# Optimization experiments

Hardware: AMD Instinct MI355X
Metric: run time of the kernel (lower is better)

Reference implementation:

```python
import jax, jax.numpy as jnp
import numpy as np

B, S, D, H = 2, 2048, 512, 8


def setup_inputs() -> dict:
    key = jax.random.key(0)
    ks = jax.random.split(key, 9)
    scale = 1.0 / np.sqrt(D)
    x = jax.random.normal(ks[0], (B, S, D), dtype=jnp.float32)
    # Per-head full-width projections, stacked over heads: [H, D, D]
    Wq = jax.random.normal(ks[1], (H, D, D), dtype=jnp.float32) * scale
    Wk = jax.random.normal(ks[2], (H, D, D), dtype=jnp.float32) * scale
    Wv = jax.random.normal(ks[3], (H, D, D), dtype=jnp.float32) * scale
    bq = jax.random.normal(ks[4], (H, D), dtype=jnp.float32) * 0.01
    bk = jax.random.normal(ks[5], (H, D), dtype=jnp.float32) * 0.01
    bv = jax.random.normal(ks[6], (H, D), dtype=jnp.float32) * 0.01
    Wo = jax.random.normal(ks[7], (H * D, D), dtype=jnp.float32) * (1.0 / np.sqrt(H * D))
    bo = jax.random.normal(ks[8], (D,), dtype=jnp.float32) * 0.01
    return {"x": x, "Wq": Wq, "bq": bq, "Wk": Wk, "bk": bk, "Wv": Wv, "bv": bv, "Wo": Wo, "bo": bo}


def reference(x, Wq, bq, Wk, bk, Wv, bv, Wo, bo):
    # Batched per-head projections: [B,S,D] x [H,D,E] -> [B,H,S,E]
    q = jnp.einsum('bsd,hde->bhse', x, Wq) + bq[None, :, None, :]
    k = jnp.einsum('bsd,hde->bhse', x, Wk) + bk[None, :, None, :]
    v = jnp.einsum('bsd,hde->bhse', x, Wv) + bv[None, :, None, :]
    # NOTE: original module has NO 1/sqrt(d) scaling
    scores = jnp.einsum('bhse,bhte->bhst', q, k)  # [B,H,S,S]
    attn = jax.nn.softmax(scores, axis=-1)
    out = jnp.einsum('bhst,bhte->bhse', attn, v)  # [B,H,S,D]
    # Concat heads along feature dim: [B,S,H*D]
    cat = out.transpose(0, 2, 1, 3).reshape(B, S, H * D)
    return cat @ Wo + bo
```

## Files before the change

kernel.cpp:

```cpp
#include <hip/hip_runtime.h>

typedef _Float16 f16;
typedef _Float16 f16x8 __attribute__((ext_vector_type(8)));
typedef float f32x4 __attribute__((ext_vector_type(4)));

#define B_ 2
#define S_ 2048
#define D_ 512
#define H_ 8

__device__ inline void async_ld16(const void* g, void* l) {
  __builtin_amdgcn_global_load_lds((__attribute__((address_space(1))) void*)(g),
                                   (__attribute__((address_space(3))) void*)(l),
                                   16, 0, 0);
}

__global__ __launch_bounds__(256) void cvt_f16(const float* __restrict__ src,
                                               f16* __restrict__ dst, long n) {
  long i = (long)blockIdx.x * 256 + threadIdx.x;
  if (i >= n) return;
  dst[i] = (f16)src[i];
}

__global__ __launch_bounds__(256) void transpose_f32(const float* __restrict__ src,
                                                     f16* __restrict__ dst, int R, int C) {
  __shared__ float t[32][33];
  size_t zoff = (size_t)blockIdx.z * R * C;
  const float* s = src + zoff;
  int tx = threadIdx.x;
  int ty = threadIdx.y;
  int c0 = blockIdx.x * 32, r0 = blockIdx.y * 32;
#pragma unroll
  for (int i = 0; i < 4; ++i)
    t[ty + i * 8][tx] = s[(size_t)(r0 + ty + i * 8) * C + c0 + tx];
  __syncthreads();
#pragma unroll
  for (int i = 0; i < 4; ++i)
    dst[zoff + (size_t)(c0 + ty + i * 8) * R + r0 + tx] = (f16)t[tx][ty + i * 8];
}

__global__ __launch_bounds__(256) void reduce_out(const float* __restrict__ part,
                                                  const float* __restrict__ bo,
                                                  float* __restrict__ out, long n, int nslab) {
  long i = (long)blockIdx.x * 256 + threadIdx.x;
  if (i >= n) return;
  float v = bo[i & (D_ - 1)];
  for (int s = 0; s < nslab; ++s) v += part[(long)s * n + i];
  out[i] = v;
}

struct GemmArgs {
  const f16 *A, *Bm;
  void* C;
  const float* bias;
  float* Mloc;
  int K, lda, ldb, ldc;
  int zbase, NG, PBG;
  long sAp, sAb, sAg, sAz;
  long sBp, sBb, sBg, sBz;
  long sCp, sCb, sCg, sCz;
  long sbp, sbb, sbg, sbz;
  long sMlz;
};

template <typename OutT, int BIAS, bool PEXP>
__global__ __launch_bounds__(256) void gemm_nt(GemmArgs p) {
  int zloc = blockIdx.z;
  int zi = p.zbase + zloc;
  int pp = zi / p.PBG; int rz = zi - pp * p.PBG;
  int bb = rz / p.NG;  int g = rz - bb * p.NG;
  const f16* A  = p.A + (pp * p.sAp + bb * p.sAb + g * p.sAg + (long)zloc * p.sAz);
  const f16* Bm = p.Bm + (pp * p.sBp + bb * p.sBb + g * p.sBg + (long)zloc * p.sBz);
  OutT* C = (OutT*)p.C + (pp * p.sCp + bb * p.sCb + g * p.sCg + (long)zloc * p.sCz);
  const float* bias = nullptr;
  if (BIAS) bias = p.bias + (pp * p.sbp + bb * p.sbb + g * p.sbg + (long)zloc * p.sbz);

  __shared__ f16 lA[4096];
  __shared__ f16 lB[4096];
  __shared__ float lMx[PEXP ? 256 : 1];

  int tid = threadIdx.x;
  int lane = tid & 63;
  int w = tid >> 6;
  int wm = (w >> 1) << 6;
  int wn = (w & 1) << 6;
  long bm = (long)blockIdx.y * 128;
  long bn = (long)blockIdx.x * 128;

  f32x4 acc[4][4] = {};
  int qd = lane >> 4;
  int fr = lane & 15;

  int q0 = tid, q1 = tid + 256;
  int r0s = q0 >> 2, c0s = (q0 & 3) ^ ((r0s >> 1) & 3);
  int r1s = q1 >> 2, c1s = (q1 & 3) ^ ((r1s >> 1) & 3);

  for (int k0 = 0; k0 < p.K; k0 += 32) {
    long oa0 = (bm + r0s) * (long)p.lda + (k0 + c0s * 8);
    long oa1 = (bm + r1s) * (long)p.lda + (k0 + c1s * 8);
    long ob0 = (bn + r0s) * (long)p.ldb + (k0 + c0s * 8);
    long ob1 = (bn + r1s) * (long)p.ldb + (k0 + c1s * 8);
    __syncthreads();
    async_ld16(A + oa0,  lA + (size_t)q0 * 8);
    async_ld16(A + oa1,  lA + (size_t)q1 * 8);
    async_ld16(Bm + ob0, lB + (size_t)q0 * 8);
    async_ld16(Bm + ob1, lB + (size_t)q1 * 8);
    __syncthreads();

    f16x8 ah[4], bh[4];
#pragma unroll
    for (int i = 0; i < 4; ++i) {
      int m = wm + i * 16 + fr;
      ah[i] = *(const f16x8*)(lA + ((size_t)m * 4 + (qd ^ ((m >> 1) & 3))) * 8);
      int n = wn + i * 16 + fr;
      bh[i] = *(const f16x8*)(lB + ((size_t)n * 4 + (qd ^ ((n >> 1) & 3))) * 8);
    }
#pragma unroll
    for (int i = 0; i < 4; ++i)
#pragma unroll
      for (int j = 0; j < 4; ++j)
        acc[i][j] = __builtin_amdgcn_mfma_f32_16x16x32_f16(ah[i], bh[j], acc[i][j], 0, 0, 0);
  }

  int rr0 = qd * 4;
  if (PEXP) {
#pragma unroll
    for (int i = 0; i < 4; ++i) {
#pragma unroll
      for (int r = 0; r < 4; ++r) {
        float v = fmaxf(fmaxf(acc[i][0][r], acc[i][1][r]),
                        fmaxf(acc[i][2][r], acc[i][3][r]));
        v = fmaxf(v, __shfl_xor(v, 1, 64));
        v = fmaxf(v, __shfl_xor(v, 2, 64));
        v = fmaxf(v, __shfl_xor(v, 4, 64));
        v = fmaxf(v, __shfl_xor(v, 8, 64));
        if (fr == 0) lMx[(w & 1) * 128 + wm + i * 16 + rr0 + r] = v;
      }
    }
    __syncthreads();
    if (tid < 128) {
      float ml = fmaxf(lMx[tid], lMx[128 + tid]);
      p.Mloc[(long)zloc * p.sMlz + (long)blockIdx.x * S_ + bm + tid] = ml;
    }
#pragma unroll
    for (int i = 0; i < 4; ++i) {
#pragma unroll
      for (int r = 0; r < 4; ++r) {
        int rl = wm + i * 16 + rr0 + r;
        float ml = fmaxf(lMx[rl], lMx[128 + rl]);
        long row = bm + rl;
#pragma unroll
        for (int j = 0; j < 4; ++j) {
          long col = bn + wn + j * 16 + fr;
          ((f16*)C)[row * (long)p.ldc + col] = (f16)__expf(acc[i][j][r] - ml);
        }
      }
    }
  } else {
#pragma unroll
    for (int i = 0; i < 4; ++i) {
#pragma unroll
      for (int j = 0; j < 4; ++j) {
#pragma unroll
        for (int r = 0; r < 4; ++r) {
          long row = bm + wm + i * 16 + rr0 + r;
          long col = bn + wn + j * 16 + fr;
          float v = acc[i][j][r];
          if (BIAS == 1) v += bias[col];
          if (BIAS == 2) v += bias[row];
          C[row * (long)p.ldc + col] = (OutT)v;
        }
      }
    }
  }
}

struct QkvArgs {
  const f16 *xh, *wqk, *wv;
  f16 *qk, *vT;
  const float *bqk, *bv;
};

template <int MH, int NH>
__device__ inline void phase_mfma(const f16* L, int cur, int qr, int qc,
                                  int qd, int fr, f32x4 (&acc)[2][2][4][2]) {
  const f16* Ab = L + cur * 32768 + MH * 8192;
  const f16* Bb = L + cur * 32768 + 16384 + NH * 8192;
  f16x8 af[4][2], bf[2][2];
#pragma unroll
  for (int i = 0; i < 4; ++i) {
    int rr = qr * 64 + i * 16 + fr;
#pragma unroll
    for (int ks = 0; ks < 2; ++ks) {
      int cc = ks * 4 + qd;
      af[i][ks] = *(const f16x8*)(Ab + ((size_t)rr * 8 + (cc ^ ((rr >> 1) & 7))) * 8);
    }
  }
#pragma unroll
  for (int j = 0; j < 2; ++j) {
    int rr = qc * 32 + j * 16 + fr;
#pragma unroll
    for (int ks = 0; ks < 2; ++ks) {
      int cc = ks * 4 + qd;
      bf[j][ks] = *(const f16x8*)(Bb + ((size_t)rr * 8 + (cc ^ ((rr >> 1) & 7))) * 8);
    }
  }
  __builtin_amdgcn_s_setprio(1);
#pragma unroll
  for (int i = 0; i < 4; ++i)
#pragma unroll
    for (int j = 0; j < 2; ++j)
#pragma unroll
      for (int ks = 0; ks < 2; ++ks)
        acc[MH][NH][i][j] = __builtin_amdgcn_mfma_f32_16x16x32_f16(
            af[i][ks], bf[j][ks], acc[MH][NH][i][j], 0, 0, 0);
  __builtin_amdgcn_s_setprio(0);
}

#define QWAIT(N)                                              \
  asm volatile("s_waitcnt vmcnt(" #N ")" ::: "memory");       \
  __builtin_amdgcn_s_barrier();                               \
  __builtin_amdgcn_sched_barrier(0);
#define QBAR()                                                \
  __builtin_amdgcn_s_barrier();                               \
  __builtin_amdgcn_sched_barrier(0);

__global__ __launch_bounds__(512, 2) void qkv_proj8(QkvArgs p) {
  const long SD = (long)S_ * D_, DD = (long)D_ * D_, DS = (long)D_ * S_;
  int zi = blockIdx.z;
  int pp = zi >> 4;
  int r = zi & 15;
  int b = r >> 3, h = r & 7;
  int bid = blockIdx.x;
  const f16 *A, *Bm;
  f16* C;
  const float* bias;
  long bm, bn;
  int ldc;
  bool biasRow;
  if (pp < 2) {
    A = p.xh + (long)b * SD;
    Bm = p.wqk + ((long)pp * 8 + h) * DD;
    C = p.qk + (long)zi * SD;
    bias = p.bqk + ((long)pp * 8 + h) * D_;
    bm = (long)(bid >> 1) * 256; bn = (long)(bid & 1) * 256;
    ldc = D_; biasRow = false;
  } else {
    A = p.wv + (long)h * DD;
    Bm = p.xh + (long)b * SD;
    C = p.vT + (long)(b * 8 + h) * DS;
    bias = p.bv + (long)h * D_;
    bm = (long)(bid >> 3) * 256; bn = (long)(bid & 7) * 256;
    ldc = S_; biasRow = true;
  }

  __shared__ f16 L[65536];

  int tid = threadIdx.x;
  int lane = tid & 63;
  int w = tid >> 6;
  int qr = w >> 2, qc = w & 3;
  int qd = lane >> 4, fr = lane & 15;

  f32x4 acc[2][2][4][2] = {};

  int srl = w * 16 + (lane >> 3);
  int sslot = lane & 7;

  auto stage = [&](const f16* src, long row0, int kb, int ldsBase) {
#pragma unroll
    for (int k = 0; k < 2; ++k) {
      int rl = srl + k * 8;
      int c = sslot ^ ((rl >> 1) & 7);
      async_ld16(src + (row0 + rl) * (long)D_ + (kb + c * 8),
                 L + ldsBase + (w * 2 + k) * 512 + lane * 8);
    }
  };
  auto iA = [&](int buf, int hh, int t) {
    stage(A, bm + hh * 128, t * 64, buf * 32768 + hh * 8192);
  };
  auto iB = [&](int buf, int hh, int t) {
    stage(Bm, bn + hh * 128, t * 64, buf * 32768 + 16384 + hh * 8192);
  };

  iA(0, 0, 0); iB(0, 0, 0); iB(0, 1, 0); iA(0, 1, 0);

  int cur = 0;
  for (int t = 0; t < 7; ++t) {
    int nxt = cur ^ 1;
    iA(nxt, 0, t + 1);
    QWAIT(6)
    phase_mfma<0, 0>(L, cur, qr, qc, qd, fr, acc);
    iB(nxt, 0, t + 1);
    QWAIT(6)
    phase_mfma<0, 1>(L, cur, qr, qc, qd, fr, acc);
    iB(nxt, 1, t + 1);
    QWAIT(6)
    phase_mfma<1, 0>(L, cur, qr, qc, qd, fr, acc);
    iA(nxt, 1, t + 1);
    QBAR()
    phase_mfma<1, 1>(L, cur, qr, qc, qd, fr, acc);
    cur = nxt;
  }
  QWAIT(4)
  phase_mfma<0, 0>(L, cur, qr, qc, qd, fr, acc);
  QWAIT(2)
  phase_mfma<0, 1>(L, cur, qr, qc, qd, fr, acc);
  QWAIT(0)
  phase_mfma<1, 0>(L, cur, qr, qc, qd, fr, acc);
  QBAR()
  phase_mfma<1, 1>(L, cur, qr, qc, qd, fr, acc);

  int rr0 = qd * 4;
#pragma unroll
  for (int mh = 0; mh < 2; ++mh)
#pragma unroll
    for (int nh = 0; nh < 2; ++nh)
#pragma unroll
      for (int i = 0; i < 4; ++i)
#pragma unroll
        for (int j = 0; j < 2; ++j)
#pragma unroll
          for (int rl = 0; rl < 4; ++rl) {
            long row = bm + mh * 128 + qr * 64 + i * 16 + rr0 + rl;
            long col = bn + nh * 128 + qc * 32 + j * 16 + fr;
            float v = acc[mh][nh][i][j][rl] + (biasRow ? bias[row] : bias[col]);
            C[row * (long)ldc + col] = (f16)v;
          }
}

struct PvArgs {
  const f16* S; const float* Ml; const f16* V; f16* C;
  int ldc, zbase, NG;
  long sVz, sCb, sCg;
};
__global__ __launch_bounds__(256) void pv_flash(PvArgs p) {
  int zloc = blockIdx.z;
  int zi = p.zbase + zloc;
  int bb = zi / p.NG; int g = zi - bb * p.NG;
  const f16* Sm = p.S + (long)zloc * S_ * S_;
  const float* Ml = p.Ml + (long)zloc * 16 * S_;
  const f16* V = p.V + (long)zloc * p.sVz;
  f16* C = p.C + bb * p.sCb + g * p.sCg;

  __shared__ f16 lP[2][64 * 32];
  __shared__ f16 lV[2][128 * 32];

  int tid = threadIdx.x;
  int lane = tid & 63;
  int w = tid >> 6;
  long bm = (long)blockIdx.y * 64;
  long bn = (long)blockIdx.x * 128;
  int e0 = (w & 1) << 6;
  int m0 = (w >> 1) << 5;

  int qd = lane >> 4;
  int fr = lane & 15;

  f32x4 acc[2][4] = {};
  f32x4 lacc[2] = {};
  f16x8 ones;
#pragma unroll
  for (int j = 0; j < 8; ++j) ones[j] = (f16)1.0f;

  float mg[2];
#pragma unroll
  for (int i = 0; i < 2; ++i) {
    float m = -1e30f;
#pragma unroll
    for (int cb = 0; cb < 16; ++cb)
      m = fmaxf(m, Ml[cb * S_ + bm + m0 + i * 16 + fr]);
    mg[i] = m;
  }
  f16 al16[2];

  int rs = tid >> 2, cs = (tid & 3) ^ ((rs >> 1) & 3);

  for (int k0 = 0; k0 < S_; k0 += 64) {
    if ((k0 & 127) == 0) {
      int cb = k0 >> 7;
#pragma unroll
      for (int i = 0; i < 2; ++i)
        al16[i] = (f16)__expf(Ml[cb * S_ + bm + m0 + i * 16 + fr] - mg[i]);
    }
    __syncthreads();
#pragma unroll
    for (int t = 0; t < 2; ++t) {
      async_ld16(Sm + (bm + rs) * (long)S_ + (k0 + t * 32 + cs * 8),
                 lP[t] + (size_t)tid * 8);
#pragma unroll
      for (int j = 0; j < 2; ++j) {
        int q = j * 256 + tid;
        int rv = q >> 2, cv = (q & 3) ^ ((rv >> 1) & 3);
        async_ld16(V + (bn + rv) * (long)S_ + (k0 + t * 32 + cv * 8),
                   lV[t] + (size_t)q * 8);
      }
    }
    __syncthreads();

#pragma unroll
    for (int t = 0; t < 2; ++t) {
      f16x8 ah[2], bh[4];
#pragma unroll
      for (int i = 0; i < 2; ++i) {
        int m = m0 + i * 16 + fr;
        ah[i] = *(const f16x8*)(lP[t] + ((size_t)m * 4 + (qd ^ ((m >> 1) & 3))) * 8);
#pragma unroll
        for (int j = 0; j < 8; ++j) ah[i][j] *= al16[i];
      }
#pragma unroll
      for (int j = 0; j < 4; ++j) {
        int n = e0 + j * 16 + fr;
        bh[j] = *(const f16x8*)(lV[t] + ((size_t)n * 4 + (qd ^ ((n >> 1) & 3))) * 8);
      }
#pragma unroll
      for (int i = 0; i < 2; ++i) {
        lacc[i] = __builtin_amdgcn_mfma_f32_16x16x32_f16(ah[i], ones, lacc[i], 0, 0, 0);
#pragma unroll
        for (int j = 0; j < 4; ++j)
          acc[i][j] = __builtin_amdgcn_mfma_f32_16x16x32_f16(ah[i], bh[j], acc[i][j], 0, 0, 0);
      }
    }
  }

  int rr0 = qd * 4;
#pragma unroll
  for (int i = 0; i < 2; ++i) {
    float inv[4];
#pragma unroll
    for (int r = 0; r < 4; ++r) inv[r] = 1.0f / lacc[i][r];
#pragma unroll
    for (int j = 0; j < 4; ++j) {
#pragma unroll
      for (int r = 0; r < 4; ++r) {
        long row = bm + m0 + i * 16 + rr0 + r;
        long col = bn + e0 + j * 16 + fr;
        C[row * (long)p.ldc + col] = (f16)(acc[i][j][r] * inv[r]);
      }
    }
  }
}

extern "C" void kernel_launch(void* const* d_in, const int* in_sizes, int n_in,
                              void* d_out, int out_size, void* d_ws, size_t ws_size,
                              hipStream_t stream) {
  const float* x  = (const float*)d_in[0];
  const float* Wq = (const float*)d_in[1];
  const float* bq = (const float*)d_in[2];
  const float* Wk = (const float*)d_in[3];
  const float* bk = (const float*)d_in[4];
  const float* Wv = (const float*)d_in[5];
  const float* bv = (const float*)d_in[6];
  const float* Wo = (const float*)d_in[7];
  const float* bo = (const float*)d_in[8];
  float* out = (float*)d_out;

  auto al = [](size_t v) { return (v + 255) & ~(size_t)255; };
  const size_t eX = (size_t)B_ * S_ * D_;
  const size_t eW = (size_t)H_ * D_ * D_;
  const size_t eSS = (size_t)S_ * S_;
  const long SD = (long)S_ * D_;
  const long DD = (long)D_ * D_;
  const long DS = (long)D_ * S_;

  size_t fixed = al(eX * 2) + al(2 * eW * 2) + al(eW * 2) + al(eW * 2)
               + al(2ULL * H_ * D_ * 4);
  int NB = 1, GH = 1, GS = 1; bool found = false;
  for (int nb = 2; nb >= 1 && !found; --nb)
    for (int gh = 8; gh >= 1 && !found; gh >>= 1)
      for (int gs = nb * gh; gs >= 1 && !found; gs >>= 1) {
        size_t need = fixed + al((size_t)nb * S_ * H_ * D_ * 2)
                    + al(2ULL * nb * gh * S_ * D_ * 2)
                    + al((size_t)nb * gh * D_ * S_ * 2)
                    + al(4ULL * nb * SD * 4)
                    + al((size_t)gs * eSS * 2)
                    + al((size_t)gs * 16 * S_ * 4);
        if (need <= ws_size) { NB = nb; GH = gh; GS = gs; found = true; }
      }

  char* p0 = (char*)d_ws;
  size_t off = 0;
  f16* xh    = (f16*)(p0 + off); off += al(eX * 2);
  f16* wqk   = (f16*)(p0 + off); off += al(2 * eW * 2);
  f16* wv    = (f16*)(p0 + off); off += al(eW * 2);
  f16* wo    = (f16*)(p0 + off); off += al(eW * 2);
  float* bqk = (float*)(p0 + off); off += al(2ULL * H_ * D_ * 4);
  f16* catb  = (f16*)(p0 + off); off += al((size_t)NB * S_ * H_ * D_ * 2);
  f16* qk    = (f16*)(p0 + off); off += al(2ULL * NB * GH * S_ * D_ * 2);
  f16* vT    = (f16*)(p0 + off); off += al((size_t)NB * GH * D_ * S_ * 2);
  float* opart = (float*)(p0 + off); off += al(4ULL * NB * SD * 4);
  f16* scores = (f16*)(p0 + off); off += al((size_t)GS * eSS * 2);
  float* mloc = (float*)(p0 + off);

  cvt_f16<<<dim3((unsigned)((eX + 255) / 256)), 256, 0, stream>>>(x, xh, (long)eX);
  dim3 tb(32, 8, 1);
  transpose_f32<<<dim3(16, 16, H_), tb, 0, stream>>>(Wq, wqk, D_, D_);
  transpose_f32<<<dim3(16, 16, H_), tb, 0, stream>>>(Wk, wqk + eW, D_, D_);
  transpose_f32<<<dim3(16, 16, H_), tb, 0, stream>>>(Wv, wv, D_, D_);
  transpose_f32<<<dim3(16, 128, 1), tb, 0, stream>>>(Wo, wo, H_ * D_, D_);
  hipMemcpyAsync(bqk, bq, (size_t)H_ * D_ * 4, hipMemcpyDeviceToDevice, stream);
  hipMemcpyAsync(bqk + H_ * D_, bk, (size_t)H_ * D_ * 4, hipMemcpyDeviceToDevice, stream);

  for (int b0 = 0; b0 < B_; b0 += NB) {
    for (int h0 = 0; h0 < H_; h0 += GH) {
      if (NB == 2 && GH == 8) {
        QkvArgs a{xh, wqk, wv, qk, vT, bqk, bv};
        qkv_proj8<<<dim3(16, 1, 48), 512, 0, stream>>>(a);
      } else {
        {
          GemmArgs a{};
          a.A = xh + (long)b0 * SD;
          a.Bm = wqk + (long)h0 * DD;
          a.C = qk; a.bias = bqk + (long)h0 * D_;
          a.K = D_; a.lda = D_; a.ldb = D_; a.ldc = D_;
          a.zbase = 0; a.NG = GH; a.PBG = NB * GH;
          a.sAb = SD;
          a.sBp = (long)H_ * DD; a.sBg = DD;
          a.sCz = SD;
          a.sbp = (long)H_ * D_; a.sbg = D_;
          gemm_nt<f16, 1, false><<<dim3(4, 16, 2 * NB * GH), 256, 0, stream>>>(a);
        }
        {
          GemmArgs a{};
          a.A = wv + (long)h0 * DD; a.Bm = xh + (long)b0 * SD;
          a.C = vT; a.bias = bv + (long)h0 * D_;
          a.K = D_; a.lda = D_; a.ldb = D_; a.ldc = S_;
          a.zbase = 0; a.NG = GH; a.PBG = NB * GH;
          a.sAg = DD;
          a.sBb = SD;
          a.sCz = DS;
          a.sbg = D_;
          gemm_nt<f16, 2, false><<<dim3(16, 4, NB * GH), 256, 0, stream>>>(a);
        }
      }
      for (int g0 = 0; g0 < NB * GH; g0 += GS) {
        {
          GemmArgs a{};
          a.A = qk + (long)g0 * SD;
          a.Bm = qk + ((long)NB * GH + g0) * SD;
          a.C = scores; a.Mloc = mloc;
          a.K = D_; a.lda = D_; a.ldb = D_; a.ldc = S_;
          a.zbase = g0; a.NG = GH; a.PBG = NB * GH;
          a.sAz = SD; a.sBz = SD; a.sCz = (long)eSS;
          a.sMlz = 16L * S_;
          gemm_nt<f16, 0, true><<<dim3(16, 16, GS), 256, 0, stream>>>(a);
        }
        {
          PvArgs a{};
          a.S = scores; a.Ml = mloc; a.V = vT + (long)g0 * DS;
          a.C = catb + (long)h0 * D_;
          a.ldc = H_ * D_; a.zbase = g0; a.NG = GH;
          a.sVz = DS; a.sCb = (long)S_ * H_ * D_; a.sCg = D_;
          pv_flash<<<dim3(4, S_ / 64, GS), 256, 0, stream>>>(a);
        }
      }
    }
    {
      GemmArgs a{};
      a.A = catb; a.Bm = wo;
      a.C = opart;
      a.K = 1024; a.lda = H_ * D_; a.ldb = H_ * D_; a.ldc = D_;
      a.zbase = 0; a.NG = 4; a.PBG = NB * 4;
      a.sAb = (long)S_ * H_ * D_; a.sAg = 1024;
      a.sBg = 1024;
      a.sCb = SD; a.sCg = (long)NB * SD;
      gemm_nt<float, 0, false><<<dim3(4, 16, NB * 4), 256, 0, stream>>>(a);
    }
    reduce_out<<<dim3((unsigned)(((long)NB * SD + 255) / 256)), 256, 0, stream>>>(
        opart, bo, out + (long)b0 * SD, (long)NB * SD, 4);
  }
}
```

Before: 488.5 us.

## Use 8-wave 256x256 tile kernel for QK^T scores with fused row-max and exp

Replaces the generic gemm_nt launch for the attention scores with a dedicated kernel using 512 threads per block and a 256x256 output tile per block. K-steps are double-buffered in shared memory, the row max is reduced across the four column waves, and exp(score - max) is written directly. The wider tile is meant to raise operand reuse and MFMA density per block, at the cost of larger LDS use (128KB plus reduction buffer) and lower occupancy. It writes the same max twice to match the existing 16-slot Ml layout.

```diff
diff --git a/kernel.cpp b/kernel.cpp
--- a/kernel.cpp
+++ b/kernel.cpp
@@ -327,6 +327,121 @@
             float v = acc[mh][nh][i][j][rl] + (biasRow ? bias[row] : bias[col]);
             C[row * (long)ldc + col] = (f16)v;
           }
+}
+
+struct Sc8Args {
+  const f16 *Q, *K;
+  f16* P;
+  float* Ml;
+};
+
+__global__ __launch_bounds__(512, 2) void scores8(Sc8Args p) {
+  int zloc = blockIdx.z;
+  const f16* A  = p.Q + (long)zloc * S_ * D_;
+  const f16* Bm = p.K + (long)zloc * S_ * D_;
+  f16* C = p.P + (long)zloc * (long)S_ * S_;
+  float* Ml = p.Ml + (long)zloc * 16L * S_;
+  int bid = blockIdx.x;
+  long bm = (long)(bid >> 3) * 256, bn = (long)(bid & 7) * 256;
+
+  __shared__ f16 L[65536];
+  __shared__ float lMx2[4][256];
+
+  int tid = threadIdx.x;
+  int lane = tid & 63;
+  int w = tid >> 6;
+  int qr = w >> 2, qc = w & 3;
+  int qd = lane >> 4, fr = lane & 15;
+
+  f32x4 acc[2][2][4][2] = {};
+
+  int srl = w * 16 + (lane >> 3);
+  int sslot = lane & 7;
+
+  auto stage = [&](const f16* src, long row0, int kb, int ldsBase) {
+#pragma unroll
+    for (int k = 0; k < 2; ++k) {
+      int rl = srl + k * 8;
+      int c = sslot ^ ((rl >> 1) & 7);
+      async_ld16(src + (row0 + rl) * (long)D_ + (kb + c * 8),
+                 L + ldsBase + (w * 2 + k) * 512 + lane * 8);
+    }
+  };
+  auto iA = [&](int buf, int hh, int t) {
+    stage(A, bm + hh * 128, t * 64, buf * 32768 + hh * 8192);
+  };
+  auto iB = [&](int buf, int hh, int t) {
+    stage(Bm, bn + hh * 128, t * 64, buf * 32768 + 16384 + hh * 8192);
+  };
+
+  iA(0, 0, 0); iB(0, 0, 0); iB(0, 1, 0); iA(0, 1, 0);
+
+  int cur = 0;
+  for (int t = 0; t < 7; ++t) {
+    int nxt = cur ^ 1;
+    iA(nxt, 0, t + 1);
+    QWAIT(6)
+    phase_mfma<0, 0>(L, cur, qr, qc, qd, fr, acc);
+    iB(nxt, 0, t + 1);
+    QWAIT(6)
+    phase_mfma<0, 1>(L, cur, qr, qc, qd, fr, acc);
+    iB(nxt, 1, t + 1);
+    QWAIT(6)
+    phase_mfma<1, 0>(L, cur, qr, qc, qd, fr, acc);
+    iA(nxt, 1, t + 1);
+    QBAR()
+    phase_mfma<1, 1>(L, cur, qr, qc, qd, fr, acc);
+    cur = nxt;
+  }
+  QWAIT(4)
+  phase_mfma<0, 0>(L, cur, qr, qc, qd, fr, acc);
+  QWAIT(2)
+  phase_mfma<0, 1>(L, cur, qr, qc, qd, fr, acc);
+  QWAIT(0)
+  phase_mfma<1, 0>(L, cur, qr, qc, qd, fr, acc);
+  QBAR()
+  phase_mfma<1, 1>(L, cur, qr, qc, qd, fr, acc);
+
+#pragma unroll
+  for (int mh = 0; mh < 2; ++mh)
+#pragma unroll
+    for (int i = 0; i < 4; ++i)
+#pragma unroll
+      for (int rl = 0; rl < 4; ++rl) {
+        float v = fmaxf(fmaxf(acc[mh][0][i][0][rl], acc[mh][0][i][1][rl]),
+                        fmaxf(acc[mh][1][i][0][rl], acc[mh][1][i][1][rl]));
+        v = fmaxf(v, __shfl_xor(v, 1, 64));
+        v = fmaxf(v, __shfl_xor(v, 2, 64));
+        v = fmaxf(v, __shfl_xor(v, 4, 64));
+        v = fmaxf(v, __shfl_xor(v, 8, 64));
+        if (fr == 0) lMx2[qc][mh * 128 + qr * 64 + i * 16 + qd * 4 + rl] = v;
+      }
+  __syncthreads();
+  if (tid < 256) {
+    float ml = fmaxf(fmaxf(lMx2[0][tid], lMx2[1][tid]),
+                     fmaxf(lMx2[2][tid], lMx2[3][tid]));
+    int cb0 = (bid & 7) * 2;
+    Ml[(long)cb0 * S_ + bm + tid] = ml;
+    Ml[(long)(cb0 + 1) * S_ + bm + tid] = ml;
+  }
+#pragma unroll
+  for (int mh = 0; mh < 2; ++mh)
+#pragma unroll
+    for (int i = 0; i < 4; ++i)
+#pragma unroll
+      for (int rl = 0; rl < 4; ++rl) {
+        int rowLoc = mh * 128 + qr * 64 + i * 16 + qd * 4 + rl;
+        float ml = fmaxf(fmaxf(lMx2[0][rowLoc], lMx2[1][rowLoc]),
+                         fmaxf(lMx2[2][rowLoc], lMx2[3][rowLoc]));
+        long row = bm + rowLoc;
+#pragma unroll
+        for (int nh = 0; nh < 2; ++nh)
+#pragma unroll
+          for (int j = 0; j < 2; ++j) {
+            long col = bn + nh * 128 + qc * 32 + j * 16 + fr;
+            C[row * (long)S_ + col] = (f16)__expf(acc[mh][nh][i][j][rl] - ml);
+          }
+      }
 }
 
 struct PvArgs {
@@ -535,15 +650,9 @@
       }
       for (int g0 = 0; g0 < NB * GH; g0 += GS) {
         {
-          GemmArgs a{};
-          a.A = qk + (long)g0 * SD;
-          a.Bm = qk + ((long)NB * GH + g0) * SD;
-          a.C = scores; a.Mloc = mloc;
-          a.K = D_; a.lda = D_; a.ldb = D_; a.ldc = S_;
-          a.zbase = g0; a.NG = GH; a.PBG = NB * GH;
-          a.sAz = SD; a.sBz = SD; a.sCz = (long)eSS;
-          a.sMlz = 16L * S_;
-          gemm_nt<f16, 0, true><<<dim3(16, 16, GS), 256, 0, stream>>>(a);
+          Sc8Args a{qk + (long)g0 * SD, qk + ((long)NB * GH + g0) * SD,
+                    scores, mloc};
+          scores8<<<dim3(64, 1, GS), 512, 0, stream>>>(a);
         }
         {
           PvArgs a{};
```

Result: faster. 458.3 us (-6.2%).
